# Kernel tuning notes

Measured on AMD Instinct MI355X. Metric: run time of the kernel, lower is better.

The kernel has to match this reference:

```python
import jax, jax.numpy as jnp
import numpy as np

THRESH = 0.7


def setup_inputs() -> dict:
    key = jax.random.key(0)
    k1, k2, k3 = jax.random.split(key, 3)
    B, A, H, W = 16, 9, 128, 128
    cla_map = jax.random.normal(k1, (B, 2 * A, H, W), dtype=jnp.float32)
    reg_map = jax.random.normal(k2, (B, 4 * A, H, W), dtype=jnp.float32)
    anchor = jax.random.uniform(k3, (H * W * A, 6), dtype=jnp.float32)
    return {"cla_map": cla_map, "reg_map": reg_map, "anchor": anchor,
            "src_info": 2048, "num_anchors": A}


def reference(cla_map, reg_map, anchor, src_info, num_anchors):
    B, _, H, W = cla_map.shape
    A = num_anchors
    S = float(src_info)

    # per-anchor 2-way softmax foreground score: channels are anchor-major pairs
    cla = cla_map.reshape(B, A, 2, H, W)
    fg = jax.nn.softmax(cla, axis=2)[:, :, 1]          # [B, A, H, W]

    # anchor lookup replicates original index: anchor[(k*W + k) * p]
    k_idx = jnp.arange(W)
    p_idx = jnp.arange(A)
    idx = (k_idx[None, :] * W + k_idx[None, :]) * p_idx[:, None]   # [A, W]
    anc = anchor[idx]                                   # [A, W, 6]
    acx = anc[..., 2][None, :, None, :]                 # -> broadcast [B,A,H,W]
    acy = anc[..., 3][None, :, None, :]
    aw = anc[..., 4][None, :, None, :]
    ah = anc[..., 5][None, :, None, :]

    # box decode (embedding): meta -> absolute cx,cy,w,h in source-image pixels
    reg = reg_map.reshape(B, A, 4, H, W)
    tx, ty, tw, th = reg[:, :, 0], reg[:, :, 1], reg[:, :, 2], reg[:, :, 3]
    cx = (tx * aw + acx) * S
    cy = (ty * ah + acy) * S
    w = jnp.exp(tw) * aw * S
    h = jnp.exp(th) * ah * S

    # data2box: center/size -> corners
    ltx = cx - w * 0.5
    lty = cy - h * 0.5
    rbx = cx + w * 0.5
    rby = cy + h * 0.5

    # keep boxes with fg > 0.7 that lie fully inside the source image
    valid = (fg > THRESH) & (ltx >= 0) & (lty >= 0) & (rbx <= S) & (rby <= S)
    m = valid.astype(cla_map.dtype)[..., None]          # [B, A, H, W, 1]

    proposal = jnp.stack([ltx, lty, rbx, rby], axis=-1) * m   # [B,A,H,W,4]
    rpn_box = (jnp.stack([cx, cy, w, h], axis=-1) / S) * m    # [B,A,H,W,4]
    # fixed-shape stand-in for the variable-length box lists: boxes + mask
    return jnp.concatenate([proposal, rpn_box, m], axis=-1)   # [B,A,H,W,9]
```

## Files before the change

### kernel.cpp

```cpp
#include <hip/hip_runtime.h>
#include <math.h>

#define NB 16
#define NA 9
#define HW 16384
#define SF 2048.0f

__global__ __launch_bounds__(256) void proposal_kernel(
    const float* __restrict__ cla,
    const float* __restrict__ reg,
    const float* __restrict__ anchor,
    float* __restrict__ out)
{
#pragma clang fp contract(off)
    const float invS = 1.0f / 2048.0f;

    __shared__ float4 tbl[128];
    __shared__ float  ob[256 * 9];

    const int tid = threadIdx.x;
    const int blk = blockIdx.x;
    const int ba  = blk >> 6;
    const int a   = ba % NA;
    const int b   = ba / NA;

    if (tid < 128) {
        const int row = tid * 129 * a;
        const float* p = anchor + (size_t)row * 6;
        float2 u = *(const float2*)(p + 2);
        float2 v = *(const float2*)(p + 4);
        tbl[tid] = make_float4(u.x, u.y, v.x, v.y);
    }

    const int g  = blk * 256 + tid;
    const int hw = g & (HW - 1);
    const int w  = tid & 127;

    const float* cb = cla + (((size_t)(b * (2 * NA) + 2 * a)) << 14) + hw;
    float c0 = cb[0];
    float c1 = cb[HW];
    const float* rb = reg + (((size_t)(b * (4 * NA) + 4 * a)) << 14) + hw;
    float tx = rb[0];
    float ty = rb[HW];
    float tw = rb[2 * HW];
    float th = rb[3 * HW];

    __syncthreads();
    float4 anc = tbl[w];
    const float acx = anc.x, acy = anc.y, aw = anc.z, ah = anc.w;

    float fg = 1.0f / (1.0f + __expf(c0 - c1));
    float ew = __expf(tw);
    float eh = __expf(th);

    float cx  = (tx * aw + acx) * SF;
    float cy  = (ty * ah + acy) * SF;
    float bw  = (ew * aw) * SF;
    float bh  = (eh * ah) * SF;
    float ltx = cx - bw * 0.5f;
    float lty = cy - bh * 0.5f;
    float rbx = cx + bw * 0.5f;
    float rby = cy + bh * 0.5f;

    const float ex = bw * 3e-4f + 1e-2f;
    const float ey = bh * 3e-4f + 1e-2f;
    bool near = (fabsf(fg - 0.7f) < 3e-4f)
              | (fabsf(ltx) < ex) | (fabsf(lty) < ey)
              | (fabsf(rbx - SF) < ex) | (fabsf(rby - SF) < ey);
    if (__builtin_expect(near, 0)) {
        float mx = fmaxf(c0, c1);
        float e0 = (float)exp((double)(c0 - mx));
        float e1 = (float)exp((double)(c1 - mx));
        fg = e1 / (e0 + e1);
        ew = (float)exp((double)tw);
        eh = (float)exp((double)th);
        cx  = (tx * aw + acx) * SF;
        cy  = (ty * ah + acy) * SF;
        bw  = (ew * aw) * SF;
        bh  = (eh * ah) * SF;
        ltx = cx - bw * 0.5f;
        lty = cy - bh * 0.5f;
        rbx = cx + bw * 0.5f;
        rby = cy + bh * 0.5f;
    }

    bool valid = (fg > 0.7f) & (ltx >= 0.0f) & (lty >= 0.0f)
               & (rbx <= SF) & (rby <= SF);
    float m = valid ? 1.0f : 0.0f;

    float* o = ob + tid * 9;
    o[0] = ltx * m;
    o[1] = lty * m;
    o[2] = rbx * m;
    o[3] = rby * m;
    o[4] = (cx * invS) * m;
    o[5] = (cy * invS) * m;
    o[6] = (bw * invS) * m;
    o[7] = (bh * invS) * m;
    o[8] = m;
    __syncthreads();

    const float4* ob4 = (const float4*)ob;
    float4* o4 = (float4*)out + (size_t)blk * 576;
    #pragma unroll
    for (int i = tid; i < 576; i += 256) o4[i] = ob4[i];
}

extern "C" void kernel_launch(void* const* d_in, const int* in_sizes, int n_in,
                              void* d_out, int out_size, void* d_ws, size_t ws_size,
                              hipStream_t stream) {
    const float* cla    = (const float*)d_in[0];
    const float* reg    = (const float*)d_in[1];
    const float* anchor = (const float*)d_in[2];

    const int total  = NB * NA * HW;
    const int blocks = total / 256;
    hipLaunchKernelGGL(proposal_kernel, dim3(blocks), dim3(256), 0, stream,
                       cla, reg, anchor, (float*)d_out);
}
```

Measured before the change: 26.85 us.

## Process four pixels per thread with float4 loads and direct vector stores

Each thread now handles four consecutive pixels, loading inputs as float4 and writing its 36 contiguous output floats directly as nine float4 stores. This removes the shared-memory staging buffer for the output and its second barrier. The anchor table is split into four separate arrays so it can be read with vector loads. The grid shrinks by a factor of four, and each thread uses more registers, which can lower occupancy. Each thread's nine stores cover a contiguous 144-byte span, but neighbouring threads write strided addresses, so store coalescing may be worse than the old shared-memory copy.

```diff
diff --git a/kernel.cpp b/kernel.cpp
--- a/kernel.cpp
+++ b/kernel.cpp
@@ -15,12 +15,12 @@
 #pragma clang fp contract(off)
     const float invS = 1.0f / 2048.0f;
 
-    __shared__ float4 tbl[128];
-    __shared__ float  ob[256 * 9];
+    __shared__ float sacx[128], sacy[128], saw[128], sah[128];
 
     const int tid = threadIdx.x;
     const int blk = blockIdx.x;
-    const int ba  = blk >> 6;
+    const int ba  = blk >> 4;
+    const int sub = blk & 15;
     const int a   = ba % NA;
     const int b   = ba / NA;
 
@@ -29,81 +29,101 @@
         const float* p = anchor + (size_t)row * 6;
         float2 u = *(const float2*)(p + 2);
         float2 v = *(const float2*)(p + 4);
-        tbl[tid] = make_float4(u.x, u.y, v.x, v.y);
+        sacx[tid] = u.x; sacy[tid] = u.y; saw[tid] = v.x; sah[tid] = v.y;
     }
 
-    const int g  = blk * 256 + tid;
-    const int hw = g & (HW - 1);
-    const int w  = tid & 127;
+    const int hw0 = (sub << 10) + (tid << 2);
+    const int w0  = hw0 & 127;
 
-    const float* cb = cla + (((size_t)(b * (2 * NA) + 2 * a)) << 14) + hw;
-    float c0 = cb[0];
-    float c1 = cb[HW];
-    const float* rb = reg + (((size_t)(b * (4 * NA) + 4 * a)) << 14) + hw;
-    float tx = rb[0];
-    float ty = rb[HW];
-    float tw = rb[2 * HW];
-    float th = rb[3 * HW];
+    const float* cb = cla + (((size_t)(b * (2 * NA) + 2 * a)) << 14) + hw0;
+    float4 vc0 = *(const float4*)cb;
+    float4 vc1 = *(const float4*)(cb + HW);
+    const float* rb = reg + (((size_t)(b * (4 * NA) + 4 * a)) << 14) + hw0;
+    float4 vtx = *(const float4*)(rb);
+    float4 vty = *(const float4*)(rb + HW);
+    float4 vtw = *(const float4*)(rb + 2 * HW);
+    float4 vth = *(const float4*)(rb + 3 * HW);
 
     __syncthreads();
-    float4 anc = tbl[w];
-    const float acx = anc.x, acy = anc.y, aw = anc.z, ah = anc.w;
+    float4 vacx = *(const float4*)&sacx[w0];
+    float4 vacy = *(const float4*)&sacy[w0];
+    float4 vaw  = *(const float4*)&saw[w0];
+    float4 vah  = *(const float4*)&sah[w0];
 
-    float fg = 1.0f / (1.0f + __expf(c0 - c1));
-    float ew = __expf(tw);
-    float eh = __expf(th);
+    const float C0[4]  = {vc0.x, vc0.y, vc0.z, vc0.w};
+    const float C1[4]  = {vc1.x, vc1.y, vc1.z, vc1.w};
+    const float TX[4]  = {vtx.x, vtx.y, vtx.z, vtx.w};
+    const float TY[4]  = {vty.x, vty.y, vty.z, vty.w};
+    const float TW[4]  = {vtw.x, vtw.y, vtw.z, vtw.w};
+    const float TH[4]  = {vth.x, vth.y, vth.z, vth.w};
+    const float ACX[4] = {vacx.x, vacx.y, vacx.z, vacx.w};
+    const float ACY[4] = {vacy.x, vacy.y, vacy.z, vacy.w};
+    const float AW[4]  = {vaw.x, vaw.y, vaw.z, vaw.w};
+    const float AH[4]  = {vah.x, vah.y, vah.z, vah.w};
 
-    float cx  = (tx * aw + acx) * SF;
-    float cy  = (ty * ah + acy) * SF;
-    float bw  = (ew * aw) * SF;
-    float bh  = (eh * ah) * SF;
-    float ltx = cx - bw * 0.5f;
-    float lty = cy - bh * 0.5f;
-    float rbx = cx + bw * 0.5f;
-    float rby = cy + bh * 0.5f;
+    float v[36];
 
-    const float ex = bw * 3e-4f + 1e-2f;
-    const float ey = bh * 3e-4f + 1e-2f;
-    bool near = (fabsf(fg - 0.7f) < 3e-4f)
-              | (fabsf(ltx) < ex) | (fabsf(lty) < ey)
-              | (fabsf(rbx - SF) < ex) | (fabsf(rby - SF) < ey);
-    if (__builtin_expect(near, 0)) {
-        float mx = fmaxf(c0, c1);
-        float e0 = (float)exp((double)(c0 - mx));
-        float e1 = (float)exp((double)(c1 - mx));
-        fg = e1 / (e0 + e1);
-        ew = (float)exp((double)tw);
-        eh = (float)exp((double)th);
-        cx  = (tx * aw + acx) * SF;
-        cy  = (ty * ah + acy) * SF;
-        bw  = (ew * aw) * SF;
-        bh  = (eh * ah) * SF;
-        ltx = cx - bw * 0.5f;
-        lty = cy - bh * 0.5f;
-        rbx = cx + bw * 0.5f;
-        rby = cy + bh * 0.5f;
+    #pragma unroll
+    for (int j = 0; j < 4; ++j) {
+        const float c0 = C0[j], c1 = C1[j];
+        const float tx = TX[j], ty = TY[j], tw = TW[j], th = TH[j];
+        const float acx = ACX[j], acy = ACY[j], aw = AW[j], ah = AH[j];
+
+        float fg = 1.0f / (1.0f + __expf(c0 - c1));
+        float ew = __expf(tw);
+        float eh = __expf(th);
+
+        float cx  = (tx * aw + acx) * SF;
+        float cy  = (ty * ah + acy) * SF;
+        float bw  = (ew * aw) * SF;
+        float bh  = (eh * ah) * SF;
+        float ltx = cx - bw * 0.5f;
+        float lty = cy - bh * 0.5f;
+        float rbx = cx + bw * 0.5f;
+        float rby = cy + bh * 0.5f;
+
+        const float ex = bw * 3e-4f + 1e-2f;
+        const float ey = bh * 3e-4f + 1e-2f;
+        bool near = (fabsf(fg - 0.7f) < 3e-4f)
+                  | (fabsf(ltx) < ex) | (fabsf(lty) < ey)
+                  | (fabsf(rbx - SF) < ex) | (fabsf(rby - SF) < ey);
+        if (__builtin_expect(near, 0)) {
+            float mx = fmaxf(c0, c1);
+            float e0 = (float)exp((double)(c0 - mx));
+            float e1 = (float)exp((double)(c1 - mx));
+            fg = e1 / (e0 + e1);
+            ew = (float)exp((double)tw);
+            eh = (float)exp((double)th);
+            cx  = (tx * aw + acx) * SF;
+            cy  = (ty * ah + acy) * SF;
+            bw  = (ew * aw) * SF;
+            bh  = (eh * ah) * SF;
+            ltx = cx - bw * 0.5f;
+            lty = cy - bh * 0.5f;
+            rbx = cx + bw * 0.5f;
+            rby = cy + bh * 0.5f;
+        }
+
+        bool valid = (fg > 0.7f) & (ltx >= 0.0f) & (lty >= 0.0f)
+                   & (rbx <= SF) & (rby <= SF);
+        float m = valid ? 1.0f : 0.0f;
+
+        v[j * 9 + 0] = ltx * m;
+        v[j * 9 + 1] = lty * m;
+        v[j * 9 + 2] = rbx * m;
+        v[j * 9 + 3] = rby * m;
+        v[j * 9 + 4] = (cx * invS) * m;
+        v[j * 9 + 5] = (cy * invS) * m;
+        v[j * 9 + 6] = (bw * invS) * m;
+        v[j * 9 + 7] = (bh * invS) * m;
+        v[j * 9 + 8] = m;
     }
 
-    bool valid = (fg > 0.7f) & (ltx >= 0.0f) & (lty >= 0.0f)
-               & (rbx <= SF) & (rby <= SF);
-    float m = valid ? 1.0f : 0.0f;
-
-    float* o = ob + tid * 9;
-    o[0] = ltx * m;
-    o[1] = lty * m;
-    o[2] = rbx * m;
-    o[3] = rby * m;
-    o[4] = (cx * invS) * m;
-    o[5] = (cy * invS) * m;
-    o[6] = (bw * invS) * m;
-    o[7] = (bh * invS) * m;
-    o[8] = m;
-    __syncthreads();
-
-    const float4* ob4 = (const float4*)ob;
-    float4* o4 = (float4*)out + (size_t)blk * 576;
+    const size_t e0 = ((size_t)ba << 14) + hw0;
+    float4* o4 = (float4*)(out + e0 * 9);
     #pragma unroll
-    for (int i = tid; i < 576; i += 256) o4[i] = ob4[i];
+    for (int k = 0; k < 9; ++k)
+        o4[k] = make_float4(v[4 * k], v[4 * k + 1], v[4 * k + 2], v[4 * k + 3]);
 }
 
 extern "C" void kernel_launch(void* const* d_in, const int* in_sizes, int n_in,
@@ -113,8 +133,7 @@
     const float* reg    = (const float*)d_in[1];
     const float* anchor = (const float*)d_in[2];
 
-    const int total  = NB * NA * HW;
-    const int blocks = total / 256;
+    const int blocks = (NB * NA * HW) / 1024;
     hipLaunchKernelGGL(proposal_kernel, dim3(blocks), dim3(256), 0, stream,
                        cla, reg, anchor, (float*)d_out);
 }
```

Result: slower. 43.18 us (+60.8%).

## Drop shared-memory staging; load anchors and write outputs directly from each thread

Applied to the files above, without the earlier changes.

Removes the LDS anchor table and the LDS output staging buffer with its two barriers. Each thread now reads its anchor row from global memory and writes its nine outputs with a stride of nine floats. The fp-contract-off pragma is narrowed to the rare recompute path, so the fast path can use fused multiply-adds. This saves shared-memory traffic and synchronisation, but the strided output stores coalesce worse than the float4 bulk copy, and changing FMA contraction on the fast path may shift rounding near the thresholds.

```diff
diff --git a/kernel.cpp b/kernel.cpp
--- a/kernel.cpp
+++ b/kernel.cpp
@@ -12,29 +12,14 @@
     const float* __restrict__ anchor,
     float* __restrict__ out)
 {
-#pragma clang fp contract(off)
     const float invS = 1.0f / 2048.0f;
 
-    __shared__ float4 tbl[128];
-    __shared__ float  ob[256 * 9];
-
-    const int tid = threadIdx.x;
-    const int blk = blockIdx.x;
-    const int ba  = blk >> 6;
-    const int a   = ba % NA;
-    const int b   = ba / NA;
-
-    if (tid < 128) {
-        const int row = tid * 129 * a;
-        const float* p = anchor + (size_t)row * 6;
-        float2 u = *(const float2*)(p + 2);
-        float2 v = *(const float2*)(p + 4);
-        tbl[tid] = make_float4(u.x, u.y, v.x, v.y);
-    }
-
-    const int g  = blk * 256 + tid;
+    const int g  = blockIdx.x * 256 + threadIdx.x;
+    const int w  = g & 127;
     const int hw = g & (HW - 1);
-    const int w  = tid & 127;
+    const int ba = g >> 14;
+    const int a  = ba % NA;
+    const int b  = ba / NA;
 
     const float* cb = cla + (((size_t)(b * (2 * NA) + 2 * a)) << 14) + hw;
     float c0 = cb[0];
@@ -45,9 +30,11 @@
     float tw = rb[2 * HW];
     float th = rb[3 * HW];
 
-    __syncthreads();
-    float4 anc = tbl[w];
-    const float acx = anc.x, acy = anc.y, aw = anc.z, ah = anc.w;
+    const int row = w * 129 * a;
+    const float* p = anchor + (size_t)row * 6;
+    float2 u = *(const float2*)(p + 2);
+    float2 vv = *(const float2*)(p + 4);
+    const float acx = u.x, acy = u.y, aw = vv.x, ah = vv.y;
 
     float fg = 1.0f / (1.0f + __expf(c0 - c1));
     float ew = __expf(tw);
@@ -68,6 +55,7 @@
               | (fabsf(ltx) < ex) | (fabsf(lty) < ey)
               | (fabsf(rbx - SF) < ex) | (fabsf(rby - SF) < ey);
     if (__builtin_expect(near, 0)) {
+#pragma clang fp contract(off)
         float mx = fmaxf(c0, c1);
         float e0 = (float)exp((double)(c0 - mx));
         float e1 = (float)exp((double)(c1 - mx));
@@ -88,7 +76,7 @@
                & (rbx <= SF) & (rby <= SF);
     float m = valid ? 1.0f : 0.0f;
 
-    float* o = ob + tid * 9;
+    float* o = out + (size_t)g * 9;
     o[0] = ltx * m;
     o[1] = lty * m;
     o[2] = rbx * m;
@@ -98,12 +86,6 @@
     o[6] = (bw * invS) * m;
     o[7] = (bh * invS) * m;
     o[8] = m;
-    __syncthreads();
-
-    const float4* ob4 = (const float4*)ob;
-    float4* o4 = (float4*)out + (size_t)blk * 576;
-    #pragma unroll
-    for (int i = tid; i < 576; i += 256) o4[i] = ob4[i];
 }
 
 extern "C" void kernel_launch(void* const* d_in, const int* in_sizes, int n_in,
@@ -113,8 +95,7 @@
     const float* reg    = (const float*)d_in[1];
     const float* anchor = (const float*)d_in[2];
 
-    const int total  = NB * NA * HW;
-    const int blocks = total / 256;
+    const int blocks = (NB * NA * HW) / 256;
     hipLaunchKernelGGL(proposal_kernel, dim3(blocks), dim3(256), 0, stream,
                        cla, reg, anchor, (float*)d_out);
 }
```

After: 31.19 us. +16.2%, slower.
